# Performance work log

Hardware: AMD Instinct MI355X
Metric: run time of the kernel (lower is better)

## Reference

```python
import jax, jax.numpy as jnp
import numpy as np
import math

D_MODEL = 256


def make_pe(h, w, d):
    # dh channels encode row index, dh channels encode column index,
    # each as interleaved sin/cos with log-spaced frequencies.
    dh = d // 2
    freqs = jnp.exp(jnp.arange(0, dh, 2, dtype=jnp.float32) * (-math.log(10000.0) / dh))  # [dh/2]
    r = jnp.arange(h, dtype=jnp.float32)[:, None] * freqs[None, :]  # [h, dh/2]
    c = jnp.arange(w, dtype=jnp.float32)[:, None] * freqs[None, :]  # [w, dh/2]
    rr = jnp.stack([jnp.sin(r), jnp.cos(r)], axis=-1).reshape(h, dh)  # interleave sin/cos
    cc = jnp.stack([jnp.sin(c), jnp.cos(c)], axis=-1).reshape(w, dh)
    pe = jnp.concatenate([
        jnp.broadcast_to(rr[:, None, :], (h, w, dh)),
        jnp.broadcast_to(cc[None, :, :], (h, w, dh)),
    ], axis=-1)  # [h, w, d]
    return pe.reshape(1, h * w, d)


def setup_inputs() -> dict:
    key = jax.random.key(0)
    h, w = 128, 128
    b = 8
    x = jax.random.normal(key, (b, h * w, D_MODEL), dtype=jnp.float32)
    return {"x": x, "h": h, "w": w}


def reference(x, h, w):
    # Dropout is identity in eval mode; the core op is PE-table generation + add.
    b, l, d = x.shape
    pe = make_pe(h, w, d)  # [1, h*w, d]
    return x + pe[:, :l]
```

## Files before the change

### kernel.cpp

```cpp
#include <hip/hip_runtime.h>
#include <math.h>


__global__ __launch_bounds__(256) void pe_add_kernel(
    const float* __restrict__ x,
    const int* __restrict__ hp,
    const int* __restrict__ wp,
    float* __restrict__ out,
    unsigned int n4)
{
    unsigned int idx = blockIdx.x * blockDim.x + threadIdx.x;
    if (idx >= n4) return;

    const unsigned int ww = (unsigned int)(*wp);
    const unsigned int hh = (unsigned int)(*hp);
    const unsigned int L  = hh * ww;

    unsigned int j = idx & 63u;
    unsigned int t = idx >> 6;
    unsigned int l = t % L;
    unsigned int row = l / ww;
    unsigned int col = l - row * ww;

    unsigned int d0 = j << 2;
    unsigned int dd = d0 & 127u;
    float pos = (float)((d0 < 128u) ? row : col);

    unsigned int m0 = dd >> 1;
    const float cstep = 0.14391156831212787f;
    float f0 = __expf(-(float)m0 * cstep);
    float f1 = __expf(-(float)(m0 + 1u) * cstep);
    float a0 = pos * f0;
    float a1 = pos * f1;

    float s0, c0, s1, c1;
    __sincosf(a0, &s0, &c0);
    __sincosf(a1, &s1, &c1);

    float4 xv = reinterpret_cast<const float4*>(x)[idx];
    float4 ov;
    ov.x = xv.x + s0;
    ov.y = xv.y + c0;
    ov.z = xv.z + s1;
    ov.w = xv.w + c1;
    reinterpret_cast<float4*>(out)[idx] = ov;
}

extern "C" void kernel_launch(void* const* d_in, const int* in_sizes, int n_in,
                              void* d_out, int out_size, void* d_ws, size_t ws_size,
                              hipStream_t stream) {
    const float* x = (const float*)d_in[0];
    const int* hp  = (const int*)d_in[1];
    const int* wp  = (const int*)d_in[2];
    float* out     = (float*)d_out;

    unsigned int n4 = (unsigned int)(out_size / 4);
    unsigned int blocks = (n4 + 255u) / 256u;
    pe_add_kernel<<<blocks, 256, 0, stream>>>(x, hp, wp, out, n4);
}
```

Baseline: 222.6 us.

## Reuse computed PE across batch with grid-stride loop and nontemporal loads/stores

```diff
diff --git a/kernel.cpp b/kernel.cpp
--- a/kernel.cpp
+++ b/kernel.cpp
@@ -1,6 +1,8 @@
 #include <hip/hip_runtime.h>
 #include <math.h>
 
+
+typedef float f32x4 __attribute__((ext_vector_type(4)));
 
 __global__ __launch_bounds__(256) void pe_add_kernel(
     const float* __restrict__ x,
@@ -9,41 +11,56 @@
     float* __restrict__ out,
     unsigned int n4)
 {
-    unsigned int idx = blockIdx.x * blockDim.x + threadIdx.x;
-    if (idx >= n4) return;
-
     const unsigned int ww = (unsigned int)(*wp);
     const unsigned int hh = (unsigned int)(*hp);
     const unsigned int L  = hh * ww;
+    const unsigned int span = L << 6;
+    if (span == 0u) return;
+    const unsigned int nb = n4 / span;
 
-    unsigned int j = idx & 63u;
-    unsigned int t = idx >> 6;
-    unsigned int l = t % L;
-    unsigned int row = l / ww;
-    unsigned int col = l - row * ww;
+    const bool wpow2 = (ww & (ww - 1u)) == 0u;
+    const unsigned int wshift = (unsigned int)__builtin_ctz(ww);
+    const unsigned int wmask  = ww - 1u;
 
-    unsigned int d0 = j << 2;
-    unsigned int dd = d0 & 127u;
-    float pos = (float)((d0 < 128u) ? row : col);
+    const float cstep = 0.14391156831212787f;
 
-    unsigned int m0 = dd >> 1;
-    const float cstep = 0.14391156831212787f;
-    float f0 = __expf(-(float)m0 * cstep);
-    float f1 = __expf(-(float)(m0 + 1u) * cstep);
-    float a0 = pos * f0;
-    float a1 = pos * f1;
+    const unsigned int stride = gridDim.x * blockDim.x;
+    for (unsigned int u = blockIdx.x * blockDim.x + threadIdx.x;
+         u < span; u += stride) {
 
-    float s0, c0, s1, c1;
-    __sincosf(a0, &s0, &c0);
-    __sincosf(a1, &s1, &c1);
+        const unsigned int j = u & 63u;
+        const unsigned int l = u >> 6;
 
-    float4 xv = reinterpret_cast<const float4*>(x)[idx];
-    float4 ov;
-    ov.x = xv.x + s0;
-    ov.y = xv.y + c0;
-    ov.z = xv.z + s1;
-    ov.w = xv.w + c1;
-    reinterpret_cast<float4*>(out)[idx] = ov;
+        unsigned int row, col;
+        if (wpow2) { row = l >> wshift; col = l & wmask; }
+        else       { row = l / ww;      col = l - row * ww; }
+
+        const unsigned int d0 = j << 2;
+        const unsigned int dd = d0 & 127u;
+        const float pos = (float)((d0 < 128u) ? row : col);
+
+        const unsigned int m0 = dd >> 1;
+        const float f0 = __expf(-(float)m0 * cstep);
+        const float f1 = __expf(-(float)(m0 + 1u) * cstep);
+
+        float s0, c0, s1, c1;
+        __sincosf(pos * f0, &s0, &c0);
+        __sincosf(pos * f1, &s1, &c1);
+
+        const f32x4* xp = reinterpret_cast<const f32x4*>(x) + u;
+        f32x4*       op = reinterpret_cast<f32x4*>(out) + u;
+
+        const f32x4 pe = { s0, c0, s1, c1 };
+
+        #pragma unroll 8
+        for (unsigned int b = 0; b < nb; ++b) {
+            f32x4 xv = __builtin_nontemporal_load(xp);
+            f32x4 ov = xv + pe;
+            __builtin_nontemporal_store(ov, op);
+            xp += span;
+            op += span;
+        }
+    }
 }
 
 extern "C" void kernel_launch(void* const* d_in, const int* in_sizes, int n_in,
@@ -54,7 +71,9 @@
     const int* wp  = (const int*)d_in[2];
     float* out     = (float*)d_out;
 
-    unsigned int n4 = (unsigned int)(out_size / 4);
+    const unsigned int n4 = (unsigned int)(out_size / 4);
+
     unsigned int blocks = (n4 + 255u) / 256u;
+    if (blocks > 2048u) blocks = 2048u;
     pe_add_kernel<<<blocks, 256, 0, stream>>>(x, hp, wp, out, n4);
 }
```

Result: slower. 240.6 us (+8.1%).
